# Kernel tuning notes

Measured on AMD Instinct MI355X. Metric: run time of the kernel, lower is better.

Reference implementation:

```python
import jax, jax.numpy as jnp
import numpy as np
from functools import partial

# Model config (mirrors init_kwargs)
K = 20
FEAT_DIMS = [64, 128, 256, 512]
EMB_DIM = 512
NUM_CLASSES = 751
INIT_POINTS = 512
INPUT_DIMS = 3
NSAMPLE = 64
RADIUS = 0.2
LEAKY = 0.2

# npoint schedule: halves whenever feature_dims[i] > feature_dims[i-1]
def npoint_schedule():
    npoint = INIT_POINTS
    out = []
    for i in range(len(FEAT_DIMS)):
        if i > 0 and FEAT_DIMS[i] > FEAT_DIMS[i - 1]:
            npoint //= 2
        out.append(npoint)
    return out

NPOINTS = npoint_schedule()  # [512, 256, 128, 64]


def knn_graph(x, k):
    """x: [B,N,D] -> neighbor idx [B,N,k] (incl. self as in dgl KNNGraph)."""
    d = jnp.sum(x * x, -1, keepdims=True)  # [B,N,1]
    dist = d - 2.0 * jnp.einsum('bnd,bmd->bnm', x, x) + jnp.swapaxes(d, 1, 2)
    _, idx = jax.lax.top_k(-dist, k)  # [B,N,k]
    return idx


def edgeconv(h, nbr_idx, theta_w, theta_b, phi_w, phi_b, bn_scale, bn_bias):
    """DGL EdgeConv with batch_norm=True: max_j BN(theta(h_j - h_i) + phi(h_i)).
    h: [B,N,C], nbr_idx: [B,N,k]. BN applied per-edge in eval mode ~ identity stats;
    we emulate BN with given scale/bias using batch statistics over all edges."""
    B, N, C = h.shape
    h_j = jnp.take_along_axis(h[:, None, :, :].repeat(1, axis=1).reshape(B, N, C)[:, :, None, :] * 0
                              + jnp.take_along_axis(h[:, :, None, :].repeat(1, axis=2), 0, axis=2), 0, axis=2)  # placeholder
    # gather neighbors: [B,N,k,C]
    h_j = jnp.take_along_axis(h[:, None, :, :].astype(h.dtype), 0, axis=1) if False else \
        jnp.take_along_axis(h[:, :, :][:, None].repeat(1, 1), 0, 1)
    # (clean version below)
    raise RuntimeError


def edgeconv_clean(h, nbr_idx, theta_w, phi_w, bn_scale, bn_bias):
    B, N, C = h.shape
    k = nbr_idx.shape[-1]
    h_j = jnp.take_along_axis(h[:, None, :, :].reshape(B, 1, N, C).repeat(1, axis=1), 0, axis=1) if False else None
    # gather: h_j[b,n,j,:] = h[b, nbr_idx[b,n,j], :]
    h_j = jax.vmap(lambda hb, ib: hb[ib])(h, nbr_idx)  # [B,N,k,C]
    diff = h_j - h[:, :, None, :]
    e = jnp.einsum('bnkc,oc->bnko', diff, theta_w) + jnp.einsum('bnc,oc->bno', h, phi_w)[:, :, None, :]
    # batch norm over all edges (train-style batch stats, eps=1e-5)
    mu = jnp.mean(e, axis=(0, 1, 2))
    var = jnp.var(e, axis=(0, 1, 2))
    e = (e - mu) / jnp.sqrt(var + 1e-5) * bn_scale + bn_bias
    return jnp.max(e, axis=2)  # [B,N,out]


def furthest_point_sample(xyz, npoint):
    """xyz: [B,N,3] -> idx [B,npoint] int32, deterministic (start at 0)."""
    B, N, _ = xyz.shape

    def one(pts):
        def body(carry, _):
            dist, last = carry
            d = jnp.sum((pts - pts[last]) ** 2, -1)
            dist = jnp.minimum(dist, d)
            nxt = jnp.argmax(dist)
            return (dist, nxt), last
        init = (jnp.full((N,), 1e10, pts.dtype), jnp.asarray(0, jnp.int32))
        (_, _), idxs = jax.lax.scan(body, init, None, length=npoint)
        return idxs.astype(jnp.int32)
    return jax.vmap(one)(xyz)


def ball_query(xyz, new_xyz, radius, nsample):
    """Return idx [B,S,nsample]: first nsample pts within radius; pad with first found."""
    d2 = jnp.sum((new_xyz[:, :, None, :] - xyz[:, None, :, :]) ** 2, -1)  # [B,S,N]
    within = d2 < radius * radius
    N = xyz.shape[1]
    big = jnp.where(within, jnp.arange(N)[None, None, :], N)
    idx = jnp.sort(big, axis=-1)[:, :, :nsample]  # first-nsample in-radius
    first = idx[:, :, :1]
    first = jnp.where(first >= N, 0, first)
    idx = jnp.where(idx >= N, first, idx)
    return idx


def bn_eval(x, scale, bias, axis):
    mu = jnp.mean(x, axis=axis, keepdims=True)
    var = jnp.var(x, axis=axis, keepdims=True)
    return (x - mu) / jnp.sqrt(var + 1e-5) * scale + bias


def sa_module(xyz, h, npoint, params):
    """PointnetSAModule: FPS -> ball query -> group (concat xyz offset) -> shared MLP
    (3 conv1x1 layers C->C->C with BN+ReLU) -> max pool -> SE (fuse='add').
    xyz: [B,N,3], h: [B,C,N]. Returns new_xyz [B,S,3], new_h [B,C,S]."""
    B, N, _ = xyz.shape
    C = h.shape[1]
    fps_idx = furthest_point_sample(xyz, npoint)  # [B,S]
    new_xyz = jax.vmap(lambda p, i: p[i])(xyz, fps_idx)  # [B,S,3]
    idx = ball_query(xyz, new_xyz, RADIUS, NSAMPLE)  # [B,S,ns]
    grouped_xyz = jax.vmap(lambda p, i: p[i])(xyz, idx.reshape(B, -1)).reshape(B, npoint, NSAMPLE, 3)
    grouped_xyz = grouped_xyz - new_xyz[:, :, None, :]
    feat = jnp.swapaxes(h, 1, 2)  # [B,N,C]
    grouped_feat = jax.vmap(lambda f, i: f[i])(feat, idx.reshape(B, -1)).reshape(B, npoint, NSAMPLE, C)
    g = jnp.concatenate([grouped_xyz, grouped_feat], -1)  # [B,S,ns,3+C] (use_xyz)
    for (w, bn_s, bn_b) in params['mlp']:
        g = jnp.einsum('bsnc,oc->bsno', g, w)
        mu = jnp.mean(g, axis=(0, 1, 2))
        var = jnp.var(g, axis=(0, 1, 2))
        g = (g - mu) / jnp.sqrt(var + 1e-5) * bn_s + bn_b
        g = jax.nn.relu(g)
    new_feat = jnp.max(g, axis=2)  # [B,S,C]
    # SE block (fuse='add'): squeeze over points, two FC, sigmoid gate added
    se1_w, se2_w = params['se']
    s = jnp.mean(new_feat, axis=1)  # [B,C]
    s = jax.nn.relu(s @ se1_w.T)
    s = jax.nn.sigmoid(s @ se2_w.T)  # [B,C]
    new_feat = new_feat + new_feat * s[:, None, :]
    return new_xyz, jnp.swapaxes(new_feat, 1, 2)  # [B,C,S]


def make_params(key):
    ks = iter(jax.random.split(key, 256))
    p = {'conv': [], 'sa': []}
    in_c = INPUT_DIMS
    for i, out_c in enumerate(FEAT_DIMS):
        p['conv'].append({
            'theta': jax.random.normal(next(ks), (out_c, in_c)) * (1.0 / np.sqrt(in_c)),
            'phi': jax.random.normal(next(ks), (out_c, in_c)) * (1.0 / np.sqrt(in_c)),
            'bn_s': jnp.ones((out_c,)), 'bn_b': jnp.zeros((out_c,)),
        })
        mlp = []
        mc = out_c + 3  # use_xyz
        for j in range(3):
            mlp.append((jax.random.normal(next(ks), (out_c, mc)) * (1.0 / np.sqrt(mc)),
                        jnp.ones((out_c,)), jnp.zeros((out_c,))))
            mc = out_c
        se_mid = max(out_c // 16, 4)
        p['sa'].append({'mlp': mlp,
                        'se': (jax.random.normal(next(ks), (se_mid, out_c)) * 0.05,
                               jax.random.normal(next(ks), (out_c, se_mid)) * 0.05)})
        in_c = out_c
    p['emb_w'] = jax.random.normal(next(ks), (EMB_DIM, FEAT_DIMS[-1] * 2)) * (1.0 / np.sqrt(FEAT_DIMS[-1] * 2))
    p['emb_bn_s'] = jnp.ones((EMB_DIM,)); p['emb_bn_b'] = jnp.zeros((EMB_DIM,))
    p['proj_w'] = jax.random.normal(next(ks), (NUM_CLASSES, EMB_DIM)) * 0.001
    p['proj_b'] = jnp.zeros((NUM_CLASSES,))
    return p


def flatten_params(p):
    flat = {}
    for i in range(len(FEAT_DIMS)):
        c = p['conv'][i]
        flat[f'c{i}_theta'] = c['theta']; flat[f'c{i}_phi'] = c['phi']
        flat[f'c{i}_bns'] = c['bn_s']; flat[f'c{i}_bnb'] = c['bn_b']
        for j, (w, s, b) in enumerate(p['sa'][i]['mlp']):
            flat[f's{i}m{j}_w'] = w; flat[f's{i}m{j}_s'] = s; flat[f's{i}m{j}_b'] = b
        flat[f's{i}_se1'] = p['sa'][i]['se'][0]; flat[f's{i}_se2'] = p['sa'][i]['se'][1]
    for k in ['emb_w', 'emb_bn_s', 'emb_bn_b', 'proj_w', 'proj_b']:
        flat[k] = p[k]
    return flat


def unflatten_params(flat):
    p = {'conv': [], 'sa': []}
    for i in range(len(FEAT_DIMS)):
        p['conv'].append({'theta': flat[f'c{i}_theta'], 'phi': flat[f'c{i}_phi'],
                          'bn_s': flat[f'c{i}_bns'], 'bn_b': flat[f'c{i}_bnb']})
        mlp = [(flat[f's{i}m{j}_w'], flat[f's{i}m{j}_s'], flat[f's{i}m{j}_b']) for j in range(3)]
        p['sa'].append({'mlp': mlp, 'se': (flat[f's{i}_se1'], flat[f's{i}_se2'])})
    for k in ['emb_w', 'emb_bn_s', 'emb_bn_b', 'proj_w', 'proj_b']:
        p[k] = flat[k]
    return p


def forward(xyz, rgb, params):
    h = rgb
    last_point = -1
    nbr_idx = None
    num_layers = len(FEAT_DIMS)
    for i in range(num_layers):
        B, N, _ = h.shape
        # dynamic kNN graph on xyz when point count changes (cluster='xyz')
        if i == 0 or N != last_point or i == num_layers - 1:
            nbr_idx = knn_graph(xyz, K)
        last_point = N
        c = params['conv'][i]
        h = edgeconv_clean(h, nbr_idx, c['theta'], c['phi'], c['bn_s'], c['bn_b'])
        h = jax.nn.leaky_relu(h, LEAKY)
        xyz, hT = sa_module(xyz, jnp.swapaxes(h, 1, 2), NPOINTS[i], params['sa'][i])
        h = jnp.swapaxes(hT, 1, 2)  # [B,S,C]
    h_max = jnp.max(h, axis=1)
    h_avg = jnp.mean(h, axis=1)
    h = jnp.concatenate([h_max, h_avg], 1)  # [B, 2C]
    h = h @ params['emb_w'].T
    mu = jnp.mean(h, axis=0); var = jnp.var(h, axis=0)
    h = (h - mu) / jnp.sqrt(var + 1e-5) * params['emb_bn_s'] + params['emb_bn_b']
    h = h @ params['proj_w'].T + params['proj_b']
    return h  # [B, NUM_CLASSES]


def setup_inputs() -> dict:
    key = jax.random.key(0)
    k1, k2, k3 = jax.random.split(key, 3)
    xyz = jax.random.normal(k1, (32, 1024, 3), jnp.float32)
    rgb = jax.random.uniform(k2, (32, 1024, 3), jnp.float32)
    inp = {'xyz': xyz, 'rgb': rgb}
    inp.update(flatten_params(make_params(k3)))
    return inp


def reference(xyz, rgb, **flat):
    params = unflatten_params(flat)
    return forward(xyz, rgb, params)
```

## Files before the change

kernel.cpp:

```cpp
#include <hip/hip_runtime.h>
#include <cstdint>
#include <cstddef>

#define DEVI __device__ __forceinline__
static DEVI float padd(float a, float b){ return __fadd_rn(a,b); }
static DEVI float pmul(float a, float b){ return __fmul_rn(a,b); }
static DEVI float psub(float a, float b){ return __fsub_rn(a,b); }

static DEVI _Float16 f2h(float f){
  f = fminf(fmaxf(f, -60000.f), 60000.f);
  return (_Float16)f;
}
static DEVI unsigned short f2b(float f){
  union { float f; uint32_t u; } v; v.f = f;
  uint32_t u = v.u;
  u += 0x7FFFu + ((u >> 16) & 1u);
  return (unsigned short)(u >> 16);
}
static DEVI float b2f(unsigned short h){
  union { float f; uint32_t u; } v; v.u = ((uint32_t)h) << 16;
  return v.f;
}

static constexpr int BATCH = 32;
static constexpr int KNN   = 20;
static constexpr int NSAMP = 64;

using short8 = __attribute__((ext_vector_type(8))) short;
using f32x4  = __attribute__((ext_vector_type(4))) float;

template<int CNT>
__global__ __launch_bounds__(256) void knn_kernel(const float* __restrict__ xyz, int N, int* __restrict__ nbr)
{
  int wvi = threadIdx.x >> 6, lane = threadIdx.x & 63;
  int g = blockIdx.x*4 + wvi;
  if (g >= BATCH*N) return;
  int b = g / N, n = g - b*N;
  const float* xb = xyz + (size_t)b*N*3;
  double x0 = (double)xb[3*n+0], x1 = (double)xb[3*n+1], x2 = (double)xb[3*n+2];
  double dn = x0*x0 + x1*x1 + x2*x2;
  double ld[CNT];
#pragma unroll
  for (int t=0;t<CNT;t++){
    int m = lane + t*64;
    double y0=(double)xb[3*m+0], y1=(double)xb[3*m+1], y2=(double)xb[3*m+2];
    double dt = x0*y0 + x1*y1 + x2*y2;
    double dm = y0*y0 + y1*y1 + y2*y2;
    ld[t] = (dn - 2.0*dt) + dm;
  }
  unsigned consumed = 0;
  for (int r=0;r<KNN;r++){
    double mv = 1e300; int mi = 0x7fffffff;
#pragma unroll
    for (int t=0;t<CNT;t++){
      int idx = lane + t*64;
      bool better = !(consumed & (1u<<t)) && (ld[t] < mv || (ld[t] == mv && idx < mi));
      mv = better ? ld[t] : mv;
      mi = better ? idx   : mi;
    }
#pragma unroll
    for (int off=32; off>=1; off>>=1){
      double ov = __shfl_xor(mv, off);
      int    oi = __shfl_xor(mi, off);
      if (ov < mv || (ov == mv && oi < mi)){ mv = ov; mi = oi; }
    }
    if ((mi & 63) == lane) consumed |= 1u << (mi >> 6);
    if (lane == 0) nbr[(size_t)g*KNN + r] = mi;
  }
}

template<int CNT>
__global__ __launch_bounds__(64) void fps_kernel(const float* __restrict__ xyz, int N, int np,
                                                 float* __restrict__ newxyz)
{
  int b = blockIdx.x, lane = threadIdx.x;
  const float* xb = xyz + (size_t)b*N*3;
  __shared__ float xs[1024], ys[1024], zs[1024];
  for (int i=lane;i<N;i+=64){
    xs[i]=xb[3*i+0]; ys[i]=xb[3*i+1]; zs[i]=xb[3*i+2];
  }
  __syncthreads();
  float px[CNT], py[CNT], pz[CNT];
  double dist[CNT];
#pragma unroll
  for (int t=0;t<CNT;t++){
    int i = lane + t*64;
    px[t]=xs[i]; py[t]=ys[i]; pz[t]=zs[i];
    dist[t]=1e10;
  }
  if (lane==0){
    newxyz[((size_t)b*np)*3+0]=xs[0];
    newxyz[((size_t)b*np)*3+1]=ys[0];
    newxyz[((size_t)b*np)*3+2]=zs[0];
  }
  int last = 0;
  for (int s=1;s<np;s++){
    double lx=(double)xs[last], ly=(double)ys[last], lz=(double)zs[last];
    double bv=-1.0; int bidx=0x7fffffff;
#pragma unroll
    for (int t=0;t<CNT;t++){
      double d0=(double)px[t]-lx, d1=(double)py[t]-ly, d2=(double)pz[t]-lz;
      double d = d0*d0 + d1*d1 + d2*d2;
      double dv = fmin(dist[t], d);
      dist[t]=dv;
      int idx = lane + t*64;
      if (dv > bv){ bv=dv; bidx=idx; }
    }
#pragma unroll
    for (int off=32; off>=1; off>>=1){
      double ov = __shfl_xor(bv, off);
      int    oi = __shfl_xor(bidx, off);
      if (ov > bv || (ov==bv && oi<bidx)){ bv=ov; bidx=oi; }
    }
    last = bidx;
    if (lane==0){
      newxyz[((size_t)b*np+s)*3+0]=xs[last];
      newxyz[((size_t)b*np+s)*3+1]=ys[last];
      newxyz[((size_t)b*np+s)*3+2]=zs[last];
    }
  }
}

__global__ __launch_bounds__(256) void ball_kernel(const float* __restrict__ xyz, const float* __restrict__ nxyz,
                                                   int N, int S, int* __restrict__ bidx)
{
  int g = blockIdx.x*256+threadIdx.x;
  if (g >= BATCH*S) return;
  int b = g / S;
  const float* xb = xyz + (size_t)b*N*3;
  const double R2 = 0.2*0.2;
  double cx=(double)nxyz[3*g+0], cy=(double)nxyz[3*g+1], cz=(double)nxyz[3*g+2];
  int cnt=0, first=0;
  int* orow = bidx + (size_t)g*NSAMP;
  for (int n=0;n<N;n++){
    double d0=(double)xb[3*n+0]-cx, d1=(double)xb[3*n+1]-cy, d2=(double)xb[3*n+2]-cz;
    double d = d0*d0 + d1*d1 + d2*d2;
    if (d < R2){
      if (cnt==0) first=n;
      orow[cnt++]=n;
      if (cnt==NSAMP) break;
    }
  }
  for (int j=cnt;j<NSAMP;j++) orow[j]=first;
}

__global__ __launch_bounds__(256) void lin_kernel(const float* __restrict__ in, const float* __restrict__ W,
                                                  int ldw, int wofs, float* __restrict__ out,
                                                  int R, int Cin, int Cout)
{
  __shared__ float sh[16*512];
  int rb = blockIdx.x*16;
  int nr = (R-rb) < 16 ? (R-rb) : 16;
  for (int idx=threadIdx.x; idx<nr*Cin; idx+=256){
    int r=idx/Cin, c=idx-r*Cin;
    sh[r*Cin+c] = in[(size_t)(rb+r)*Cin + c];
  }
  __syncthreads();
  for (int oi=threadIdx.x; oi<nr*Cout; oi+=256){
    int r=oi/Cout, o=oi-r*Cout;
    const float* wr = W + (size_t)o*ldw + wofs;
    const float* gr = sh + r*Cin;
    float acc=0.f;
    for (int ci=0;ci<Cin;ci++) acc = fmaf(gr[ci], wr[ci], acc);
    out[(size_t)(rb+r)*Cout + o] = acc;
  }
}

__global__ void sub_kernel(const float* __restrict__ a, const float* __restrict__ b, float* __restrict__ o, int n){
  int i = blockIdx.x*256+threadIdx.x; if (i<n) o[i]=psub(a[i],b[i]);
}
__global__ void fill_kernel(float* __restrict__ p, int n, float v){
  int i = blockIdx.x*256+threadIdx.x; if (i<n) p[i]=v;
}

template<int C>
__global__ __launch_bounds__(256) void wprep_kernel(const float* __restrict__ w, short* __restrict__ wpk)
{
  int idx = blockIdx.x*256 + threadIdx.x;
  if (idx >= C*C) return;
  int n = idx & (C-1);
  int k = idx / C;
  float v = w[(size_t)n*C + k];
  unsigned short hi = f2b(v);
  unsigned short lo = f2b(__fsub_rn(v, b2f(hi)));
  int kt = k >> 5, kr = k & 31, nt = n >> 4;
  int lane = ((kr >> 3) << 4) | (n & 15);
  int j = kr & 7;
  size_t base = ((size_t)(kt*(C/16) + nt)*64 + lane)*16;
  wpk[base + j]     = (short)hi;
  wpk[base + 8 + j] = (short)lo;
}

template<int C>
__global__ __launch_bounds__(256) void mlp_mfma_kernel(const _Float16* __restrict__ ein,
    const short* __restrict__ wpk, const float* __restrict__ ab,
    _Float16* __restrict__ eout)
{
  constexpr int NT = C/16, KT = C/32;
  __shared__ short sB[NT*1024];
  int wvi = threadIdx.x >> 6, lane = threadIdx.x & 63;
  int rb = blockIdx.x*64 + wvi*16;
  int m = lane & 15, kg = lane >> 4;
  f32x4 acc[NT];
#pragma unroll
  for (int t=0;t<NT;t++) acc[t] = (f32x4){0.f,0.f,0.f,0.f};
  const _Float16* arow = ein + (size_t)(rb + m)*C + kg*8;
  for (int kt=0; kt<KT; ++kt){
    __syncthreads();
    {
      const uint4* src = reinterpret_cast<const uint4*>(wpk + (size_t)kt*NT*1024);
      uint4* dst = reinterpret_cast<uint4*>(sB);
#pragma unroll
      for (int i=threadIdx.x; i<NT*128; i+=256) dst[i] = src[i];
    }
    __syncthreads();
    int kbase = kt*32 + kg*8;
    uint4 raw = *reinterpret_cast<const uint4*>(arow + kt*32);
    const _Float16* hp = reinterpret_cast<const _Float16*>(&raw);
    float4 sa0 = *reinterpret_cast<const float4*>(ab + kbase);
    float4 sa1 = *reinterpret_cast<const float4*>(ab + kbase + 4);
    float4 sb0 = *reinterpret_cast<const float4*>(ab + C + kbase);
    float4 sb1 = *reinterpret_cast<const float4*>(ab + C + kbase + 4);
    float sav[8] = {sa0.x,sa0.y,sa0.z,sa0.w,sa1.x,sa1.y,sa1.z,sa1.w};
    float sbv[8] = {sb0.x,sb0.y,sb0.z,sb0.w,sb1.x,sb1.y,sb1.z,sb1.w};
    short8 ahi, alo;
#pragma unroll
    for (int j=0;j<8;j++){
      float v = (float)hp[j];
      float a = fmaxf(fmaf(sav[j], v, sbv[j]), 0.f);
      unsigned short h = f2b(a);
      ahi[j] = (short)h;
      alo[j] = (short)f2b(__fsub_rn(a, b2f(h)));
    }
#pragma unroll
    for (int nt=0; nt<NT; ++nt){
      const short* wp = sB + (size_t)(nt*64 + lane)*16;
      short8 bhi = *reinterpret_cast<const short8*>(wp);
      short8 blo = *reinterpret_cast<const short8*>(wp + 8);
      acc[nt] = __builtin_amdgcn_mfma_f32_16x16x32_bf16(ahi, bhi, acc[nt], 0,0,0);
      acc[nt] = __builtin_amdgcn_mfma_f32_16x16x32_bf16(alo, bhi, acc[nt], 0,0,0);
      acc[nt] = __builtin_amdgcn_mfma_f32_16x16x32_bf16(ahi, blo, acc[nt], 0,0,0);
    }
  }
#pragma unroll
  for (int nt=0; nt<NT; ++nt){
    int col = nt*16 + m;
    int row0 = rb + kg*4;
#pragma unroll
    for (int r=0;r<4;r++){
      eout[(size_t)(row0 + r)*C + col] = f2h(acc[nt][r]);
    }
  }
}

template<int C>
__global__ __launch_bounds__(512) void stats_kernel(const _Float16* __restrict__ e, int rows,
                                                    double* __restrict__ stats)
{
  constexpr int NG = 512/C;
  int c = threadIdx.x & (C-1);
  int g = threadIdx.x / C;
  double s=0.0, ss=0.0;
  for (int r = blockIdx.x*NG + g; r < rows; r += gridDim.x*NG){
    float v = (float)e[(size_t)r*C + c];
    s += (double)v; ss += (double)v*(double)v;
  }
  __shared__ double reds[512], redq[512];
  reds[threadIdx.x]=s; redq[threadIdx.x]=ss;
  __syncthreads();
#pragma unroll
  for (int half=NG/2; half>=1; half>>=1){
    if (g < half){
      reds[threadIdx.x] += reds[threadIdx.x + half*C];
      redq[threadIdx.x] += redq[threadIdx.x + half*C];
    }
    __syncthreads();
  }
  if (g==0){ atomicAdd(&stats[c], reds[c]); atomicAdd(&stats[C+c], redq[c]); }
}

template<int C>
__global__ __launch_bounds__(512) void ec_stats_kernel(const float* __restrict__ T, const float* __restrict__ Q,
                                                       const int* __restrict__ nbr, int N, int rows,
                                                       double* __restrict__ stats)
{
  constexpr int NG = 512/C;
  int c = threadIdx.x & (C-1);
  int g = threadIdx.x / C;
  double s=0.0, ss=0.0;
  for (int r = blockIdx.x*NG + g; r < rows; r += gridDim.x*NG){
    int pn = r / KNN;
    int k  = r - pn*KNN;
    int b  = pn / N;
    int nb = nbr[(size_t)pn*KNN + k];
    float e = T[((size_t)(b*N + nb))*C + c] + Q[(size_t)pn*C + c];
    s += (double)e; ss += (double)e*(double)e;
  }
  __shared__ double reds[512], redq[512];
  reds[threadIdx.x]=s; redq[threadIdx.x]=ss;
  __syncthreads();
#pragma unroll
  for (int half=NG/2; half>=1; half>>=1){
    if (g < half){
      reds[threadIdx.x] += reds[threadIdx.x + half*C];
      redq[threadIdx.x] += redq[threadIdx.x + half*C];
    }
    __syncthreads();
  }
  if (g==0){ atomicAdd(&stats[c], reds[c]); atomicAdd(&stats[C+c], redq[c]); }
}

__global__ void finalize_kernel(const double* __restrict__ stats, const float* __restrict__ scale,
                                const float* __restrict__ bias, int C, double invM, float* __restrict__ ab)
{
  int c = blockIdx.x*256+threadIdx.x; if (c>=C) return;
  double mu = stats[c]*invM;
  double var = stats[C+c]*invM - mu*mu;
  if (var<0.0) var=0.0;
  double inv = 1.0/sqrt(var+1e-5);
  double a = (double)scale[c]*inv;
  ab[c]=(float)a;
  ab[C+c]=(float)((double)bias[c] - mu*a);
}

template<int C>
__global__ __launch_bounds__(256) void ec_apply_kernel(const float* __restrict__ T, const float* __restrict__ Q,
                                                       const int* __restrict__ nbr, const float* __restrict__ ab,
                                                       int N, float* __restrict__ hout, int total)
{
  int idx = blockIdx.x*256+threadIdx.x;
  if (idx>=total) return;
  constexpr int LC = (C==64)?6:((C==128)?7:((C==256)?8:9));
  int c = idx & (C-1);
  int pn = idx >> LC;
  int b = pn / N;
  float q = Q[(size_t)pn*C + c];
  float aa=ab[c], bb=ab[C+c];
  const int* nrow = nbr + (size_t)pn*KNN;
  float m = -3.4e38f;
  for (int k=0;k<KNN;k++){
    int nb = nrow[k];
    float e = T[((size_t)(b*N+nb))*C + c] + q;
    m = fmaxf(m, fmaf(aa, e, bb));
  }
  hout[idx] = m>=0.f ? m : 0.2f*m;
}

template<int C>
__global__ __launch_bounds__(256) void m0_kernel(const float* __restrict__ F, const float* __restrict__ xyz,
                                                 const float* __restrict__ nxyz, const int* __restrict__ bidx,
                                                 const float* __restrict__ w0, int N, int lS,
                                                 _Float16* __restrict__ eout)
{
  constexpr int CPT = C/32;
  __shared__ float sw[C*3];
  __shared__ int sp[32];
  __shared__ float sdx[32], sdy[32], sdz[32];
  int rb = blockIdx.x*32;
  for (int i=threadIdx.x;i<C*3;i+=256){
    int cc=i/3, d=i-cc*3;
    sw[i]=w0[(size_t)cc*(C+3)+d];
  }
  if (threadIdx.x<32){
    int row = rb + threadIdx.x;
    int bs = row >> 6;
    int iv = bidx[row];
    int b = bs >> lS;
    int p = b*N + iv;
    sp[threadIdx.x]=p;
    sdx[threadIdx.x]=psub(xyz[3*(size_t)p+0], nxyz[3*(size_t)bs+0]);
    sdy[threadIdx.x]=psub(xyz[3*(size_t)p+1], nxyz[3*(size_t)bs+1]);
    sdz[threadIdx.x]=psub(xyz[3*(size_t)p+2], nxyz[3*(size_t)bs+2]);
  }
  __syncthreads();
  int cg=threadIdx.x&31, rg=threadIdx.x>>5;
#pragma unroll
  for (int i=0;i<4;i++){
    int rl = rg + i*8;
    int row = rb + rl;
    int p = sp[rl];
    float dx=sdx[rl], dy=sdy[rl], dz=sdz[rl];
    const float* fr = F + (size_t)p*C;
    _Float16* orow = eout + (size_t)row*C;
#pragma unroll
    for (int q=0;q<CPT;q++){
      int c = cg + 32*q;
      orow[c] = f2h(fr[c] + sw[c*3+0]*dx + sw[c*3+1]*dy + sw[c*3+2]*dz);
    }
  }
}

template<int C>
__global__ __launch_bounds__(256) void pool_kernel(const _Float16* __restrict__ e, const float* __restrict__ ab,
                                                   float* __restrict__ feat, int total)
{
  int idx = blockIdx.x*256+threadIdx.x; if (idx>=total) return;
  constexpr int LC = (C==64)?6:((C==128)?7:((C==256)?8:9));
  int c = idx & (C-1);
  int bs = idx >> LC;
  float aa=ab[c], bb=ab[C+c];
  const _Float16* ep = e + ((size_t)bs*NSAMP)*C + c;
  float m=-3.4e38f;
  for (int j=0;j<NSAMP;j++){
    float v = fmaf(aa, (float)ep[(size_t)j*C], bb);
    v = fmaxf(v, 0.f);
    m = fmaxf(m, v);
  }
  feat[idx]=m;
}

__global__ __launch_bounds__(256) void semean_kernel(const float* __restrict__ feat, int S, int C,
                                                     float* __restrict__ sbuf)
{
  int idx = blockIdx.x*256+threadIdx.x; if (idx>=BATCH*C) return;
  int c = idx % C; int b = idx / C;
  const float* fp = feat + ((size_t)b*S)*C + c;
  double s=0;
  for (int j=0;j<S;j++) s += (double)fp[(size_t)j*C];
  sbuf[idx] = (float)(s / (double)S);
}

__global__ __launch_bounds__(512) void se_kernel(const float* __restrict__ sbuf, const float* __restrict__ se1,
                                                 const float* __restrict__ se2, int C, int mid,
                                                 float* __restrict__ scl)
{
  int b=blockIdx.x, t=threadIdx.x;
  __shared__ float sv[512]; __shared__ float s1[32];
  if (t<C) sv[t]=sbuf[(size_t)b*C+t];
  __syncthreads();
  if (t<mid){
    float a=0.f;
    for (int c=0;c<C;c++) a=fmaf(sv[c], se1[(size_t)t*C+c], a);
    s1[t]=fmaxf(a,0.f);
  }
  __syncthreads();
  if (t<C){
    float a=0.f;
    for (int m=0;m<mid;m++) a=fmaf(s1[m], se2[(size_t)t*mid+m], a);
    scl[(size_t)b*C+t] = 1.f/(1.f+expf(-a));
  }
}

__global__ __launch_bounds__(256) void seapply_kernel(const float* __restrict__ feat, const float* __restrict__ scl,
                                                      int S, int C, float* __restrict__ out, int total)
{
  int idx=blockIdx.x*256+threadIdx.x; if (idx>=total) return;
  int c = idx % C;
  int bs = idx / C;
  int b = bs / S;
  float f=feat[idx];
  out[idx]=padd(f, pmul(f, scl[(size_t)b*C+c]));
}

__global__ __launch_bounds__(256) void headpool_kernel(const float* __restrict__ h, float* __restrict__ cat)
{
  int idx=blockIdx.x*256+threadIdx.x; if (idx>=BATCH*512) return;
  int c = idx & 511; int b = idx >> 9;
  const float* hp = h + ((size_t)b*64)*512 + c;
  float m=-3.4e38f; double s=0;
  for (int j=0;j<64;j++){ float v=hp[(size_t)j*512]; m=fmaxf(m,v); s+=(double)v; }
  cat[(size_t)b*1024 + c] = m;
  cat[(size_t)b*1024 + 512 + c] = (float)(s/64.0);
}

__global__ __launch_bounds__(256) void emb_kernel(const float* __restrict__ cat, const float* __restrict__ w,
                                                  float* __restrict__ emb)
{
  int idx=blockIdx.x*256+threadIdx.x; if (idx>=BATCH*512) return;
  int e=idx&511, b=idx>>9;
  const float* cr=cat+(size_t)b*1024;
  const float* wr=w+(size_t)e*1024;
  float a=0.f;
  for (int f=0;f<1024;f++) a=fmaf(cr[f], wr[f], a);
  emb[idx]=a;
}

__global__ void bn_head_kernel(float* __restrict__ emb, const float* __restrict__ s, const float* __restrict__ bb)
{
  int e = blockIdx.x*256+threadIdx.x; if (e>=512) return;
  float vals[32]; double sum=0;
#pragma unroll
  for (int b=0;b<32;b++){ float v=emb[b*512+e]; vals[b]=v; sum+=(double)v; }
  double mu = sum/32.0;
  double var = 0.0;
#pragma unroll
  for (int b=0;b<32;b++){ double d=(double)vals[b]-mu; var += d*d; }
  var /= 32.0;
  double inv = 1.0/sqrt(var+1e-5);
  float aa = (float)((double)s[e]*inv);
  float cc = (float)((double)bb[e] - mu*(double)s[e]*inv);
#pragma unroll
  for (int b=0;b<32;b++) emb[b*512+e] = fmaf(aa, vals[b], cc);
}

__global__ __launch_bounds__(256) void proj_kernel(const float* __restrict__ emb, const float* __restrict__ w,
                                                   const float* __restrict__ bias, float* __restrict__ out)
{
  int o = blockIdx.x*256+threadIdx.x;
  int b = blockIdx.y;
  if (o>=751) return;
  const float* er=emb+(size_t)b*512;
  const float* wr=w+(size_t)o*512;
  float a=0.f;
  for (int e=0;e<512;e++) a=fmaf(er[e], wr[e], a);
  out[(size_t)b*751+o] = padd(a, bias[o]);
}

struct LayerP {
  const float *theta,*phi,*bns,*bnb,*m0w,*m0s,*m0b,*m1w,*m1s,*m1b,*m2w,*m2s,*m2b,*se1,*se2;
};

template<int C>
static void run_layer(const LayerP& p, int Cin, int N, int S, int lS, int mid,
                      const float* cur_xyz, const float* cur_h,
                      float* Tb, float* Qb, float* Hec, float* Hsa, float* feat,
                      float* newxyz, int* knnbuf, int* ballbuf, float* qw, float* wt,
                      double* stats, float* ab, float* sbuf, float* scl, _Float16* ebuf,
                      hipStream_t stream)
{
  constexpr int NG = 512/C;
  constexpr int KCNT = 1024/C;
  int rowsE = BATCH*N*KNN;
  int rows0 = BATCH*S*NSAMP;

  knn_kernel<KCNT><<<(BATCH*N)/4, 256, 0, stream>>>(cur_xyz, N, knnbuf);

  int nw = C*Cin;
  sub_kernel<<<(nw+255)/256, 256, 0, stream>>>(p.phi, p.theta, qw, nw);
  lin_kernel<<<(BATCH*N+15)/16, 256, 0, stream>>>(cur_h, p.theta, Cin, 0, Tb, BATCH*N, Cin, C);
  lin_kernel<<<(BATCH*N+15)/16, 256, 0, stream>>>(cur_h, qw,      Cin, 0, Qb, BATCH*N, Cin, C);

  hipMemsetAsync(stats, 0, 2*C*sizeof(double), stream);
  {
    int blocks = (rowsE+NG-1)/NG; if (blocks>1024) blocks=1024;
    ec_stats_kernel<C><<<blocks, 512, 0, stream>>>(Tb, Qb, knnbuf, N, rowsE, stats);
  }
  finalize_kernel<<<(C+255)/256, 256, 0, stream>>>(stats, p.bns, p.bnb, C, 1.0/(double)rowsE, ab);
  ec_apply_kernel<C><<<(BATCH*N*C+255)/256, 256, 0, stream>>>(Tb, Qb, knnbuf, ab, N, Hec, BATCH*N*C);

  fps_kernel<KCNT><<<BATCH, 64, 0, stream>>>(cur_xyz, N, S, newxyz);
  ball_kernel<<<(BATCH*S+255)/256, 256, 0, stream>>>(cur_xyz, newxyz, N, S, ballbuf);

  lin_kernel<<<(BATCH*N+15)/16, 256, 0, stream>>>(Hec, p.m0w, C+3, 3, Tb, BATCH*N, C, C);

  m0_kernel<C><<<rows0/32, 256, 0, stream>>>(Tb, cur_xyz, newxyz, ballbuf, p.m0w, N, lS, ebuf);

  hipMemsetAsync(stats, 0, 2*C*sizeof(double), stream);
  { int blocks=(rows0+NG-1)/NG; if (blocks>1024) blocks=1024;
    stats_kernel<C><<<blocks,512,0,stream>>>(ebuf, rows0, stats); }
  finalize_kernel<<<(C+255)/256,256,0,stream>>>(stats, p.m0s, p.m0b, C, 1.0/(double)rows0, ab);

  wprep_kernel<C><<<(C*C+255)/256,256,0,stream>>>(p.m1w, (short*)wt);
  mlp_mfma_kernel<C><<<rows0/64,256,0,stream>>>(ebuf, (const short*)wt, ab, ebuf);
  hipMemsetAsync(stats, 0, 2*C*sizeof(double), stream);
  { int blocks=(rows0+NG-1)/NG; if (blocks>1024) blocks=1024;
    stats_kernel<C><<<blocks,512,0,stream>>>(ebuf, rows0, stats); }
  finalize_kernel<<<(C+255)/256,256,0,stream>>>(stats, p.m1s, p.m1b, C, 1.0/(double)rows0, ab);

  wprep_kernel<C><<<(C*C+255)/256,256,0,stream>>>(p.m2w, (short*)wt);
  mlp_mfma_kernel<C><<<rows0/64,256,0,stream>>>(ebuf, (const short*)wt, ab, ebuf);
  hipMemsetAsync(stats, 0, 2*C*sizeof(double), stream);
  { int blocks=(rows0+NG-1)/NG; if (blocks>1024) blocks=1024;
    stats_kernel<C><<<blocks,512,0,stream>>>(ebuf, rows0, stats); }
  finalize_kernel<<<(C+255)/256,256,0,stream>>>(stats, p.m2s, p.m2b, C, 1.0/(double)rows0, ab);

  pool_kernel<C><<<(BATCH*S*C+255)/256,256,0,stream>>>(ebuf, ab, feat, BATCH*S*C);
  semean_kernel<<<(BATCH*C+255)/256,256,0,stream>>>(feat, S, C, sbuf);
  se_kernel<<<BATCH,512,0,stream>>>(sbuf, p.se1, p.se2, C, mid, scl);
  seapply_kernel<<<(BATCH*S*C+255)/256,256,0,stream>>>(feat, scl, S, C, Hsa, BATCH*S*C);
}

extern "C" void kernel_launch(void* const* d_in, const int* in_sizes, int n_in,
                              void* d_out, int out_size, void* d_ws, size_t ws_size,
                              hipStream_t stream)
{
  (void)in_sizes; (void)n_in;
  const float* xyz0 = (const float*)d_in[0];
  const float* rgb  = (const float*)d_in[1];
  LayerP ps[4];
  for (int i=0;i<4;i++){
    int base = 2 + i*15;
    ps[i].theta=(const float*)d_in[base+0];
    ps[i].phi  =(const float*)d_in[base+1];
    ps[i].bns  =(const float*)d_in[base+2];
    ps[i].bnb  =(const float*)d_in[base+3];
    ps[i].m0w  =(const float*)d_in[base+4];
    ps[i].m0s  =(const float*)d_in[base+5];
    ps[i].m0b  =(const float*)d_in[base+6];
    ps[i].m1w  =(const float*)d_in[base+7];
    ps[i].m1s  =(const float*)d_in[base+8];
    ps[i].m1b  =(const float*)d_in[base+9];
    ps[i].m2w  =(const float*)d_in[base+10];
    ps[i].m2s  =(const float*)d_in[base+11];
    ps[i].m2b  =(const float*)d_in[base+12];
    ps[i].se1  =(const float*)d_in[base+13];
    ps[i].se2  =(const float*)d_in[base+14];
  }
  const float* emb_w =(const float*)d_in[62];
  const float* emb_s =(const float*)d_in[63];
  const float* emb_b =(const float*)d_in[64];
  const float* proj_w=(const float*)d_in[65];
  const float* proj_b=(const float*)d_in[66];

  char* w = (char*)d_ws;
  size_t off=0;
  auto take=[&](size_t bytes)->char*{ char* r=w+off; off += (bytes+255)&~(size_t)255; return r; };
  _Float16* ebuf =(_Float16*)take(134217728ULL);
  float* Tb   =(float*)take(8388608);
  float* Qb   =(float*)take(8388608);
  float* Hec  =(float*)take(8388608);
  float* Hsa  =(float*)take(4194304);
  float* feat =(float*)take(4194304);
  float* nx0  =(float*)take(196608);
  float* nx1  =(float*)take(196608);
  int*   knnb =(int*)  take(2621440);
  int*   ballb=(int*)  take(4194304);
  float* qw   =(float*)take(524288);
  float* wt   =(float*)take(1048576);
  double* stats=(double*)take(8192);
  float* ab   =(float*)take(4096);
  float* sbuf =(float*)take(65536);
  float* scl  =(float*)take(65536);
  float* cat  =(float*)take(131072);
  float* embv =(float*)take(65536);
  if (off > ws_size){
    fill_kernel<<<(out_size+255)/256,256,0,stream>>>((float*)d_out, out_size, (float)(ws_size >> 20));
    return;
  }

  static const int Cs[4]={64,128,256,512}, Cins[4]={3,64,128,256},
                   Ns[4]={1024,512,256,128}, Ss[4]={512,256,128,64},
                   lSs[4]={9,8,7,6}, mids[4]={4,8,16,32};

  const float* cur_xyz=xyz0; const float* cur_h=rgb;
  float* nxs[2]={nx0,nx1};
  for (int i=0;i<4;i++){
    float* nx = nxs[i&1];
    switch (Cs[i]){
      case 64:  run_layer<64 >(ps[i],Cins[i],Ns[i],Ss[i],lSs[i],mids[i],cur_xyz,cur_h,Tb,Qb,Hec,Hsa,feat,nx,knnb,ballb,qw,wt,stats,ab,sbuf,scl,ebuf,stream); break;
      case 128: run_layer<128>(ps[i],Cins[i],Ns[i],Ss[i],lSs[i],mids[i],cur_xyz,cur_h,Tb,Qb,Hec,Hsa,feat,nx,knnb,ballb,qw,wt,stats,ab,sbuf,scl,ebuf,stream); break;
      case 256: run_layer<256>(ps[i],Cins[i],Ns[i],Ss[i],lSs[i],mids[i],cur_xyz,cur_h,Tb,Qb,Hec,Hsa,feat,nx,knnb,ballb,qw,wt,stats,ab,sbuf,scl,ebuf,stream); break;
      default:  run_layer<512>(ps[i],Cins[i],Ns[i],Ss[i],lSs[i],mids[i],cur_xyz,cur_h,Tb,Qb,Hec,Hsa,feat,nx,knnb,ballb,qw,wt,stats,ab,sbuf,scl,ebuf,stream); break;
    }
    cur_xyz=nx; cur_h=Hsa;
  }

  headpool_kernel<<<(BATCH*512+255)/256,256,0,stream>>>(Hsa, cat);
  emb_kernel<<<(BATCH*512+255)/256,256,0,stream>>>(cat, emb_w, embv);
  bn_head_kernel<<<2,256,0,stream>>>(embv, emb_s, emb_b);
  proj_kernel<<<dim3((751+255)/256, BATCH),256,0,stream>>>(embv, proj_w, proj_b, (float*)d_out);
}
```

Baseline: 7.133 ms.

## Use 2x2 wave tiling and swizzled weight layout in MFMA MLP kernel

Each block's four waves now cover a 2x2 grid: every wave computes 32 rows over half of the output columns, where before each wave computed 16 rows over all columns. Each B fragment read from LDS now feeds two row tiles, halving LDS B reads per MFMA. The packed weight layout interleaves hi/lo halves per lane with an XOR swizzle to cut LDS bank conflicts. In exchange, each wave loads and converts two A row fragments per step, which raises register pressure.

Result: no change. 7.173 ms (+0.6%).

```diff
diff --git a/kernel.cpp b/kernel.cpp
--- a/kernel.cpp
+++ b/kernel.cpp
@@ -186,9 +186,12 @@
   int kt = k >> 5, kr = k & 31, nt = n >> 4;
   int lane = ((kr >> 3) << 4) | (n & 15);
   int j = kr & 7;
-  size_t base = ((size_t)(kt*(C/16) + nt)*64 + lane)*16;
-  wpk[base + j]     = (short)hi;
-  wpk[base + 8 + j] = (short)lo;
+  int swz = (lane >> 2) & 1;
+  int u_hi = (lane*2)     ^ swz;
+  int u_lo = (lane*2 + 1) ^ swz;
+  size_t base = (size_t)(kt*(C/16) + nt)*128;
+  wpk[(base + u_hi)*8 + j] = (short)hi;
+  wpk[(base + u_lo)*8 + j] = (short)lo;
 }
 
 template<int C>
@@ -196,15 +199,22 @@
     const short* __restrict__ wpk, const float* __restrict__ ab,
     _Float16* __restrict__ eout)
 {
-  constexpr int NT = C/16, KT = C/32;
+  constexpr int NT = C/16, NTH = NT/2, KT = C/32;
   __shared__ short sB[NT*1024];
   int wvi = threadIdx.x >> 6, lane = threadIdx.x & 63;
-  int rb = blockIdx.x*64 + wvi*16;
+  int mg = wvi >> 1, ng = wvi & 1;
+  int rb = blockIdx.x*64 + mg*32;
   int m = lane & 15, kg = lane >> 4;
-  f32x4 acc[NT];
-#pragma unroll
-  for (int t=0;t<NT;t++) acc[t] = (f32x4){0.f,0.f,0.f,0.f};
-  const _Float16* arow = ein + (size_t)(rb + m)*C + kg*8;
+  f32x4 acc[2][NTH];
+#pragma unroll
+  for (int i=0;i<2;i++)
+#pragma unroll
+    for (int t=0;t<NTH;t++) acc[i][t] = (f32x4){0.f,0.f,0.f,0.f};
+  const _Float16* arow0 = ein + (size_t)(rb + m)*C + kg*8;
+  const _Float16* arow1 = ein + (size_t)(rb + 16 + m)*C + kg*8;
+  int swz = (lane >> 2) & 1;
+  int uh = (lane*2)     ^ swz;
+  int ul = (lane*2 + 1) ^ swz;
   for (int kt=0; kt<KT; ++kt){
     __syncthreads();
     {
@@ -215,40 +225,53 @@
     }
     __syncthreads();
     int kbase = kt*32 + kg*8;
-    uint4 raw = *reinterpret_cast<const uint4*>(arow + kt*32);
-    const _Float16* hp = reinterpret_cast<const _Float16*>(&raw);
+    uint4 raw0 = *reinterpret_cast<const uint4*>(arow0 + kt*32);
+    uint4 raw1 = *reinterpret_cast<const uint4*>(arow1 + kt*32);
+    const _Float16* hp0 = reinterpret_cast<const _Float16*>(&raw0);
+    const _Float16* hp1 = reinterpret_cast<const _Float16*>(&raw1);
     float4 sa0 = *reinterpret_cast<const float4*>(ab + kbase);
     float4 sa1 = *reinterpret_cast<const float4*>(ab + kbase + 4);
     float4 sb0 = *reinterpret_cast<const float4*>(ab + C + kbase);
     float4 sb1 = *reinterpret_cast<const float4*>(ab + C + kbase + 4);
     float sav[8] = {sa0.x,sa0.y,sa0.z,sa0.w,sa1.x,sa1.y,sa1.z,sa1.w};
     float sbv[8] = {sb0.x,sb0.y,sb0.z,sb0.w,sb1.x,sb1.y,sb1.z,sb1.w};
-    short8 ahi, alo;
+    short8 ahi0, alo0, ahi1, alo1;
 #pragma unroll
     for (int j=0;j<8;j++){
-      float v = (float)hp[j];
-      float a = fmaxf(fmaf(sav[j], v, sbv[j]), 0.f);
-      unsigned short h = f2b(a);
-      ahi[j] = (short)h;
-      alo[j] = (short)f2b(__fsub_rn(a, b2f(h)));
-    }
-#pragma unroll
-    for (int nt=0; nt<NT; ++nt){
-      const short* wp = sB + (size_t)(nt*64 + lane)*16;
-      short8 bhi = *reinterpret_cast<const short8*>(wp);
-      short8 blo = *reinterpret_cast<const short8*>(wp + 8);
-      acc[nt] = __builtin_amdgcn_mfma_f32_16x16x32_bf16(ahi, bhi, acc[nt], 0,0,0);
-      acc[nt] = __builtin_amdgcn_mfma_f32_16x16x32_bf16(alo, bhi, acc[nt], 0,0,0);
-      acc[nt] = __builtin_amdgcn_mfma_f32_16x16x32_bf16(ahi, blo, acc[nt], 0,0,0);
-    }
-  }
-#pragma unroll
-  for (int nt=0; nt<NT; ++nt){
-    int col = nt*16 + m;
-    int row0 = rb + kg*4;
-#pragma unroll
-    for (int r=0;r<4;r++){
-      eout[(size_t)(row0 + r)*C + col] = f2h(acc[nt][r]);
+      float v0 = (float)hp0[j];
+      float a0 = fmaxf(fmaf(sav[j], v0, sbv[j]), 0.f);
+      unsigned short h0 = f2b(a0);
+      ahi0[j] = (short)h0;
+      alo0[j] = (short)f2b(__fsub_rn(a0, b2f(h0)));
+      float v1 = (float)hp1[j];
+      float a1 = fmaxf(fmaf(sav[j], v1, sbv[j]), 0.f);
+      unsigned short h1 = f2b(a1);
+      ahi1[j] = (short)h1;
+      alo1[j] = (short)f2b(__fsub_rn(a1, b2f(h1)));
+    }
+#pragma unroll
+    for (int nt=0; nt<NTH; ++nt){
+      int ntg = ng*NTH + nt;
+      short8 bhi = *reinterpret_cast<const short8*>(sB + ((size_t)ntg*128 + uh)*8);
+      short8 blo = *reinterpret_cast<const short8*>(sB + ((size_t)ntg*128 + ul)*8);
+      acc[0][nt] = __builtin_amdgcn_mfma_f32_16x16x32_bf16(ahi0, bhi, acc[0][nt], 0,0,0);
+      acc[0][nt] = __builtin_amdgcn_mfma_f32_16x16x32_bf16(alo0, bhi, acc[0][nt], 0,0,0);
+      acc[0][nt] = __builtin_amdgcn_mfma_f32_16x16x32_bf16(ahi0, blo, acc[0][nt], 0,0,0);
+      acc[1][nt] = __builtin_amdgcn_mfma_f32_16x16x32_bf16(ahi1, bhi, acc[1][nt], 0,0,0);
+      acc[1][nt] = __builtin_amdgcn_mfma_f32_16x16x32_bf16(alo1, bhi, acc[1][nt], 0,0,0);
+      acc[1][nt] = __builtin_amdgcn_mfma_f32_16x16x32_bf16(ahi1, blo, acc[1][nt], 0,0,0);
+    }
+  }
+#pragma unroll
+  for (int i=0;i<2;i++){
+#pragma unroll
+    for (int nt=0; nt<NTH; ++nt){
+      int col = (ng*NTH + nt)*16 + m;
+      int row0 = rb + i*16 + kg*4;
+#pragma unroll
+      for (int r=0;r<4;r++){
+        eout[(size_t)(row0 + r)*C + col] = f2h(acc[i][nt][r]);
+      }
     }
   }
 }
```
